# Kernel optimization log

Measured on AMD Instinct MI355X. Metric: run time of the kernel, lower is better.

The kernel has to match this reference:

```python
import jax, jax.numpy as jnp
import numpy as np

D, NH = 1024, 16
B, L = 2, 2048
NEG = -1e9


def setup_inputs() -> dict:
    key = jax.random.key(0)
    ks = jax.random.split(key, 6)
    x = jax.random.normal(ks[0], (B, L, D), dtype=jnp.float32)
    # causal additive mask, broadcast over batch and heads
    causal = jnp.tril(jnp.ones((L, L), dtype=jnp.float32))
    mask = jnp.where(causal == 1.0, 0.0, NEG)[None, None, :, :]
    wx_w = jax.random.normal(ks[1], (3 * D, D), dtype=jnp.float32) * 0.02
    wx_b = jnp.zeros((3 * D,), dtype=jnp.float32)
    wo_w = jax.random.normal(ks[2], (D, D), dtype=jnp.float32) * 0.02
    wo_b = jnp.zeros((D,), dtype=jnp.float32)
    ln_g = jnp.ones((D,), dtype=jnp.float32)
    ln_b = jnp.zeros((D,), dtype=jnp.float32)
    return {"x": x, "mask": mask, "wx_w": wx_w, "wx_b": wx_b,
            "wo_w": wo_w, "wo_b": wo_b, "ln_g": ln_g, "ln_b": ln_b}


def _layernorm(x, g, b, eps=1e-5):
    mu = jnp.mean(x, axis=-1, keepdims=True)
    var = jnp.mean((x - mu) ** 2, axis=-1, keepdims=True)
    return (x - mu) * jax.lax.rsqrt(var + eps) * g + b


def reference(x, mask, wx_w, wx_b, wo_w, wo_b, ln_g, ln_b):
    b, l, d = x.shape
    nh = NH
    dh = d // nh
    h = _layernorm(x, ln_g, ln_b)
    proj = h @ wx_w.T + wx_b                       # [b, l, 3d]
    # 'b l (n nh dh) -> n b nh l dh'
    proj = proj.reshape(b, l, 3, nh, dh)
    q, k, v = jnp.moveaxis(proj, 2, 0).transpose(0, 1, 3, 2, 4)  # each [b, nh, l, dh]
    qkT = jnp.einsum('bhic,bhjc->bhij', q, k) + mask
    scale = jnp.asarray(d, jnp.float32) ** 0.5     # NOTE: sqrt(d), not sqrt(dh)
    attn = jax.nn.softmax(qkT / scale, axis=-1)
    heads = jnp.einsum('bhij,bhjc->bhic', attn, v)  # [b, nh, l, dh]
    heads = heads.transpose(0, 2, 1, 3).reshape(b, l, d)
    attention = heads @ wo_w.T + wo_b
    out = jax.nn.gelu(x + attention, approximate=False)
    return (out, mask)
```

## Files before the change

kernel.cpp:

```cpp
#include <hip/hip_runtime.h>
#include <hip/hip_bf16.h>
#include <math.h>

constexpr int kD  = 1024;
constexpr int kB  = 2;
constexpr int kL  = 2048;
constexpr int kM  = kB * kL;

typedef __attribute__((ext_vector_type(8))) short  bf8v;
typedef __attribute__((ext_vector_type(4))) float  f4v;
typedef __attribute__((ext_vector_type(4))) unsigned short us4v;

#define MFMA_BF16 __builtin_amdgcn_mfma_f32_16x16x32_bf16

__device__ inline unsigned short f2bf(float f) {
    __hip_bfloat16 h = __float2bfloat16(f);
    return *(unsigned short*)&h;
}
__device__ inline float bf2f(unsigned short u) {
    __hip_bfloat16 h = *(__hip_bfloat16*)&u;
    return __bfloat162float(h);
}
__device__ inline void gload16(const void* g, void* l) {
    __builtin_amdgcn_global_load_lds(
        (const __attribute__((address_space(1))) void*)g,
        (__attribute__((address_space(3))) void*)l, 16, 0, 0);
}

__global__ __launch_bounds__(256) void convert_split(
    const float* __restrict__ src, unsigned short* __restrict__ hi,
    unsigned short* __restrict__ lo, int n4)
{
    const int i = blockIdx.x * 256 + threadIdx.x;
    if (i >= n4) return;
    const float4 v = ((const float4*)src)[i];
    const float vv[4] = {v.x, v.y, v.z, v.w};
    us4v h, l;
    #pragma unroll
    for (int c = 0; c < 4; ++c) {
        h[c] = f2bf(vv[c]);
        l[c] = f2bf(vv[c] - bf2f(h[c]));
    }
    *(us4v*)&hi[(size_t)i * 4] = h;
    *(us4v*)&lo[(size_t)i * 4] = l;
}

__global__ __launch_bounds__(256) void ln_kernel(
    const float* __restrict__ x, const float* __restrict__ g,
    const float* __restrict__ beta, unsigned short* __restrict__ h_hi,
    unsigned short* __restrict__ h_lo)
{
    const int row = blockIdx.x;
    const int tid = threadIdx.x;
    const float4 v = ((const float4*)(x + (size_t)row * kD))[tid];
    float s  = v.x + v.y + v.z + v.w;
    float s2 = v.x*v.x + v.y*v.y + v.z*v.z + v.w*v.w;
    #pragma unroll
    for (int off = 32; off > 0; off >>= 1) {
        s  += __shfl_down(s, off);
        s2 += __shfl_down(s2, off);
    }
    __shared__ float wsum[4], wsum2[4];
    const int lane = tid & 63, wid = tid >> 6;
    if (lane == 0) { wsum[wid] = s; wsum2[wid] = s2; }
    __syncthreads();
    const float ts   = wsum[0] + wsum[1] + wsum[2] + wsum[3];
    const float ts2  = wsum2[0] + wsum2[1] + wsum2[2] + wsum2[3];
    const float mean = ts * (1.0f / kD);
    const float var  = ts2 * (1.0f / kD) - mean * mean;
    const float rstd = rsqrtf(var + 1e-5f);
    const float4 gv = ((const float4*)g)[tid];
    const float4 bv = ((const float4*)beta)[tid];
    float o[4];
    o[0] = (v.x - mean) * rstd * gv.x + bv.x;
    o[1] = (v.y - mean) * rstd * gv.y + bv.y;
    o[2] = (v.z - mean) * rstd * gv.z + bv.z;
    o[3] = (v.w - mean) * rstd * gv.w + bv.w;
    us4v h, l;
    #pragma unroll
    for (int c = 0; c < 4; ++c) {
        h[c] = f2bf(o[c]);
        l[c] = f2bf(o[c] - bf2f(h[c]));
    }
    *(us4v*)&h_hi[(size_t)row * kD + tid * 4] = h;
    *(us4v*)&h_lo[(size_t)row * kD + tid * 4] = l;
}

template<int MODE>
__global__ __launch_bounds__(256, 3) void gemm_split(
    const unsigned short* __restrict__ Ahi, const unsigned short* __restrict__ Alo,
    const unsigned short* __restrict__ Bhi, const unsigned short* __restrict__ Blo,
    const float* __restrict__ bias, const float* __restrict__ resid,
    unsigned short* __restrict__ outb, unsigned short* __restrict__ vT,
    float* __restrict__ outf, int N, int K)
{
    constexpr int NARR = (MODE == 0) ? 4 : 3;
    __shared__ unsigned short S[NARR][128][32];
    const int tid = threadIdx.x;
    const int l = tid & 63, w = tid >> 6;
    const int col16 = l & 15, grp = l >> 4;
    const int wr = (w >> 1) * 64, wc = (w & 1) * 64;
    const int row0 = blockIdx.y * 128, col0 = blockIdx.x * 128;
    const int sr = l >> 2;
    const int sc8 = ((l & 3) ^ ((sr >> 1) & 3)) * 8;
    const unsigned short* gb;
    int rb;
    if (MODE == 0) {
        gb = (w == 0) ? Ahi : (w == 1) ? Alo : (w == 2) ? Bhi : Blo;
        rb = (w < 2) ? row0 : col0;
    } else {
        gb = (w == 0) ? Ahi : (w == 1) ? Bhi : Blo;
        rb = (w == 0) ? row0 : col0;
    }
    const bool do_stage = (MODE == 0) || (w < 3);
    const int pos8 = (grp ^ ((col16 >> 1) & 3)) * 8;
    f4v acc[4][4] = {};

    for (int k0 = 0; k0 < K; k0 += 32) {
        __syncthreads();
        if (do_stage) {
            #pragma unroll
            for (int t = 0; t < 8; ++t)
                gload16(gb + (size_t)(rb + t*16 + sr) * K + k0 + sc8,
                        &S[w][t*16][0]);
        }
        __syncthreads();
        bf8v ah[4], al[4], bh[4], bl[4];
        #pragma unroll
        for (int mi = 0; mi < 4; ++mi) {
            ah[mi] = *(bf8v*)&S[0][wr + mi*16 + col16][pos8];
            if (MODE == 0) al[mi] = *(bf8v*)&S[1][wr + mi*16 + col16][pos8];
        }
        #pragma unroll
        for (int ni = 0; ni < 4; ++ni) {
            bh[ni] = *(bf8v*)&S[(MODE == 0) ? 2 : 1][wc + ni*16 + col16][pos8];
            bl[ni] = *(bf8v*)&S[(MODE == 0) ? 3 : 2][wc + ni*16 + col16][pos8];
        }
        #pragma unroll
        for (int mi = 0; mi < 4; ++mi)
            #pragma unroll
            for (int ni = 0; ni < 4; ++ni) {
                acc[mi][ni] = MFMA_BF16(ah[mi], bh[ni], acc[mi][ni], 0, 0, 0);
                acc[mi][ni] = MFMA_BF16(ah[mi], bl[ni], acc[mi][ni], 0, 0, 0);
                if (MODE == 0)
                    acc[mi][ni] = MFMA_BF16(al[mi], bh[ni], acc[mi][ni], 0, 0, 0);
            }
    }
    #pragma unroll
    for (int mi = 0; mi < 4; ++mi)
        #pragma unroll
        for (int ni = 0; ni < 4; ++ni) {
            const int gcol = col0 + wc + ni*16 + col16;
            const float bb = bias[gcol];
            #pragma unroll
            for (int rr = 0; rr < 4; ++rr) {
                const int grow = row0 + wr + mi*16 + grp*4 + rr;
                float o = acc[mi][ni][rr] + bb;
                if (MODE == 0) {
                    if (gcol < 2048) {
                        if (gcol < 1024) o *= (1.0f / 32.0f);
                        outb[(size_t)grow * 3072 + gcol] = f2bf(o);
                    } else {
                        const int dg = gcol - 2048;
                        vT[((size_t)((grow >> 11) * 16 + (dg >> 6)) * 64 + (dg & 63)) * 2048
                           + (grow & 2047)] = f2bf(o);
                    }
                } else {
                    o += resid[(size_t)grow * N + gcol];
                    o = 0.5f * o * (1.0f + erff(o * 0.70710678118654752f));
                    outf[(size_t)grow * N + gcol] = o;
                }
            }
        }
}

__global__ __launch_bounds__(256, 4) void attn_mfma(
    const unsigned short* __restrict__ projb, const unsigned short* __restrict__ vT,
    unsigned short* __restrict__ heads_hi)
{
    __shared__ unsigned short Ks[64 * 64];
    __shared__ unsigned short Vs[64 * 64];
    __shared__ unsigned int   Ps32[4][16][68];
    const int tid = threadIdx.x;
    const int l = tid & 63, w = tid >> 6;
    const int col16 = l & 15, grp = l >> 4;
    const int bh = blockIdx.x, b = bh >> 4, hh = bh & 15;
    const int qt = 31 - (int)blockIdx.y;
    const int q0 = qt * 64;
    const unsigned short* vTh = vT + (size_t)bh * 64 * 2048;

    const int r8 = l >> 3;
    const int sc8 = ((l & 7) ^ r8) * 8;
    const int isV = w >> 1;
    const int t0 = (w & 1) * 4;
    const int sw7 = col16 & 7;

    const size_t qbase = (size_t)(b*kL + q0 + w*16 + col16) * 3072 + hh*64 + grp*8;
    bf8v aq[2];
    aq[0] = *(const bf8v*)&projb[qbase];
    aq[1] = *(const bf8v*)&projb[qbase + 32];

    f4v accO[4] = {};
    float m_r[4], l_r[4];
    #pragma unroll
    for (int r = 0; r < 4; ++r) { m_r[r] = -INFINITY; l_r[r] = 0.0f; }

    for (int jt = 0; jt <= qt; ++jt) {
        const int j0 = jt * 64;
        __syncthreads();
        #pragma unroll
        for (int t2 = 0; t2 < 4; ++t2) {
            const int t = t0 + t2;
            if (isV)
                gload16(&vTh[(size_t)(t*8 + r8) * 2048 + j0 + sc8], &Vs[t*8*64]);
            else
                gload16(&projb[(size_t)(b*kL + j0 + t*8 + r8) * 3072 + hh*64 + 1024 + sc8],
                        &Ks[t*8*64]);
        }
        __syncthreads();

        f4v accS[4] = {};
        #pragma unroll
        for (int kk = 0; kk < 2; ++kk)
            #pragma unroll
            for (int nj = 0; nj < 4; ++nj) {
                const int row = nj*16 + col16;
                const bf8v bk = *(bf8v*)&Ks[row*64 + (((grp + kk*4) ^ sw7) * 8)];
                accS[nj] = MFMA_BF16(aq[kk], bk, accS[nj], 0, 0, 0);
            }

        const bool diag = (jt == qt);
        float p[4][4];
        float alpha[4];
        #pragma unroll
        for (int r = 0; r < 4; ++r) {
            const int q_local = w*16 + grp*4 + r;
            float sv[4];
            #pragma unroll
            for (int nj = 0; nj < 4; ++nj) {
                sv[nj] = accS[nj][r];
                if (diag && (nj*16 + col16 > q_local)) sv[nj] = -1e9f;
            }
            float pm = fmaxf(fmaxf(sv[0], sv[1]), fmaxf(sv[2], sv[3]));
            pm = fmaxf(pm, __shfl_xor(pm, 1));
            pm = fmaxf(pm, __shfl_xor(pm, 2));
            pm = fmaxf(pm, __shfl_xor(pm, 4));
            pm = fmaxf(pm, __shfl_xor(pm, 8));
            const float m_new = fmaxf(m_r[r], pm);
            alpha[r] = __expf(m_r[r] - m_new);
            m_r[r] = m_new;
            float ps = 0.0f;
            #pragma unroll
            for (int nj = 0; nj < 4; ++nj) {
                p[nj][r] = __expf(sv[nj] - m_new);
                ps += p[nj][r];
            }
            ps += __shfl_xor(ps, 1);
            ps += __shfl_xor(ps, 2);
            ps += __shfl_xor(ps, 4);
            ps += __shfl_xor(ps, 8);
            l_r[r] = l_r[r] * alpha[r] + ps;
        }
        #pragma unroll
        for (int nd = 0; nd < 4; ++nd)
            #pragma unroll
            for (int r = 0; r < 4; ++r)
                accO[nd][r] *= alpha[r];

        #pragma unroll
        for (int nj = 0; nj < 4; ++nj)
            #pragma unroll
            for (int r = 0; r < 4; ++r) {
                const unsigned hi = f2bf(p[nj][r]);
                const unsigned lo = f2bf(p[nj][r] - bf2f((unsigned short)hi));
                Ps32[w][grp*4 + r][nj*16 + col16] = hi | (lo << 16);
            }
        asm volatile("s_waitcnt lgkmcnt(0)" ::: "memory");

        #pragma unroll
        for (int js = 0; js < 2; ++js) {
            const uint4 pa0 = *(const uint4*)&Ps32[w][col16][js*32 + grp*8];
            const uint4 pa1 = *(const uint4*)&Ps32[w][col16][js*32 + grp*8 + 4];
            const unsigned pu[8] = {pa0.x, pa0.y, pa0.z, pa0.w,
                                    pa1.x, pa1.y, pa1.z, pa1.w};
            bf8v ph, pl;
            #pragma unroll
            for (int i = 0; i < 8; ++i) {
                ph[i] = (short)(pu[i] & 0xffffu);
                pl[i] = (short)(pu[i] >> 16);
            }
            #pragma unroll
            for (int nd = 0; nd < 4; ++nd) {
                const int row = nd*16 + col16;
                const bf8v bv = *(bf8v*)&Vs[row*64 + (((grp + js*4) ^ sw7) * 8)];
                accO[nd] = MFMA_BF16(ph, bv, accO[nd], 0, 0, 0);
                accO[nd] = MFMA_BF16(pl, bv, accO[nd], 0, 0, 0);
            }
        }
    }
    #pragma unroll
    for (int nd = 0; nd < 4; ++nd)
        #pragma unroll
        for (int r = 0; r < 4; ++r) {
            const float o = accO[nd][r] / l_r[r];
            heads_hi[(size_t)(b*kL + q0 + w*16 + grp*4 + r) * kD
                     + hh*64 + nd*16 + col16] = f2bf(o);
        }
}

extern "C" void kernel_launch(void* const* d_in, const int* in_sizes, int n_in,
                              void* d_out, int out_size, void* d_ws, size_t ws_size,
                              hipStream_t stream)
{
    const float* x    = (const float*)d_in[0];
    const float* mask = (const float*)d_in[1];
    const float* wx_w = (const float*)d_in[2];
    const float* wx_b = (const float*)d_in[3];
    const float* wo_w = (const float*)d_in[4];
    const float* wo_b = (const float*)d_in[5];
    const float* ln_g = (const float*)d_in[6];
    const float* ln_b = (const float*)d_in[7];
    float* out = (float*)d_out;

    unsigned short* h_hi  = (unsigned short*)d_ws;
    unsigned short* h_lo  = h_hi  + (size_t)kM * kD;
    unsigned short* wxhi  = h_lo  + (size_t)kM * kD;
    unsigned short* wxlo  = wxhi  + (size_t)3 * kD * kD;
    unsigned short* wohi  = wxlo  + (size_t)3 * kD * kD;
    unsigned short* wolo  = wohi  + (size_t)kD * kD;
    unsigned short* projb = wolo  + (size_t)kD * kD;
    unsigned short* hd_hi = projb + (size_t)kM * 3 * kD;
    unsigned short* vT    = hd_hi + (size_t)kM * kD;

    convert_split<<<(3*kD*kD/4 + 255)/256, 256, 0, stream>>>(wx_w, wxhi, wxlo, 3*kD*kD/4);
    convert_split<<<(kD*kD/4 + 255)/256, 256, 0, stream>>>(wo_w, wohi, wolo, kD*kD/4);
    ln_kernel<<<kM, 256, 0, stream>>>(x, ln_g, ln_b, h_hi, h_lo);
    gemm_split<0><<<dim3(3*kD/128, kM/128), 256, 0, stream>>>(
        h_hi, h_lo, wxhi, wxlo, wx_b, nullptr, projb, vT, nullptr, 3*kD, kD);
    attn_mfma<<<dim3(kB*16, kL/64), 256, 0, stream>>>(projb, vT, hd_hi);
    gemm_split<1><<<dim3(kD/128, kM/128), 256, 0, stream>>>(
        hd_hi, nullptr, wohi, wolo, wo_b, x, nullptr, nullptr, out, kD, kD);
    hipMemcpyAsync(out + (size_t)kM * kD, mask, (size_t)kL * kL * sizeof(float),
                   hipMemcpyDeviceToDevice, stream);
}
```

Baseline: 314.2 us.

## Double GEMM K-tile to 64 and use 128-row query tiles in attention

The split-bf16 GEMM now stages 64-wide K slices per barrier pair, which halves the number of sync/load rounds and changes the LDS swizzle to an 8-way XOR pattern. Occupancy for the QKV GEMM is lowered because it now uses more shared memory. The attention kernel switches to 512-thread blocks covering 128 query rows, so each staged K/V tile is shared by 8 waves instead of 4. Waves whose rows lie entirely before the last key tile skip that tile. The trade-off is fewer resident blocks and larger per-block LDS, plus coarser causal load balance.

```diff
diff --git a/kernel.cpp b/kernel.cpp
--- a/kernel.cpp
+++ b/kernel.cpp
@@ -87,7 +87,7 @@
 }
 
 template<int MODE>
-__global__ __launch_bounds__(256, 3) void gemm_split(
+__global__ __launch_bounds__(256, (MODE == 0) ? 2 : 3) void gemm_split(
     const unsigned short* __restrict__ Ahi, const unsigned short* __restrict__ Alo,
     const unsigned short* __restrict__ Bhi, const unsigned short* __restrict__ Blo,
     const float* __restrict__ bias, const float* __restrict__ resid,
@@ -95,14 +95,14 @@
     float* __restrict__ outf, int N, int K)
 {
     constexpr int NARR = (MODE == 0) ? 4 : 3;
-    __shared__ unsigned short S[NARR][128][32];
+    __shared__ unsigned short S[NARR][128][64];
     const int tid = threadIdx.x;
     const int l = tid & 63, w = tid >> 6;
     const int col16 = l & 15, grp = l >> 4;
     const int wr = (w >> 1) * 64, wc = (w & 1) * 64;
     const int row0 = blockIdx.y * 128, col0 = blockIdx.x * 128;
-    const int sr = l >> 2;
-    const int sc8 = ((l & 3) ^ ((sr >> 1) & 3)) * 8;
+    const int sr8 = l >> 3;
+    const int sc8 = ((l & 7) ^ sr8) * 8;
     const unsigned short* gb;
     int rb;
     if (MODE == 0) {
@@ -113,38 +113,42 @@
         rb = (w == 0) ? row0 : col0;
     }
     const bool do_stage = (MODE == 0) || (w < 3);
-    const int pos8 = (grp ^ ((col16 >> 1) & 3)) * 8;
+    const int sw7 = col16 & 7;
     f4v acc[4][4] = {};
 
-    for (int k0 = 0; k0 < K; k0 += 32) {
+    for (int k0 = 0; k0 < K; k0 += 64) {
         __syncthreads();
         if (do_stage) {
             #pragma unroll
-            for (int t = 0; t < 8; ++t)
-                gload16(gb + (size_t)(rb + t*16 + sr) * K + k0 + sc8,
-                        &S[w][t*16][0]);
+            for (int t = 0; t < 16; ++t)
+                gload16(gb + (size_t)(rb + t*8 + sr8) * K + k0 + sc8,
+                        &S[w][t*8][0]);
         }
         __syncthreads();
-        bf8v ah[4], al[4], bh[4], bl[4];
         #pragma unroll
-        for (int mi = 0; mi < 4; ++mi) {
-            ah[mi] = *(bf8v*)&S[0][wr + mi*16 + col16][pos8];
-            if (MODE == 0) al[mi] = *(bf8v*)&S[1][wr + mi*16 + col16][pos8];
-        }
-        #pragma unroll
-        for (int ni = 0; ni < 4; ++ni) {
-            bh[ni] = *(bf8v*)&S[(MODE == 0) ? 2 : 1][wc + ni*16 + col16][pos8];
-            bl[ni] = *(bf8v*)&S[(MODE == 0) ? 3 : 2][wc + ni*16 + col16][pos8];
-        }
-        #pragma unroll
-        for (int mi = 0; mi < 4; ++mi)
+        for (int kk = 0; kk < 2; ++kk) {
+            const int pos8 = ((grp + kk*4) ^ sw7) * 8;
+            bf8v ah[4], al[4], bh[4], bl[4];
+            #pragma unroll
+            for (int mi = 0; mi < 4; ++mi) {
+                ah[mi] = *(bf8v*)&S[0][wr + mi*16 + col16][pos8];
+                if (MODE == 0) al[mi] = *(bf8v*)&S[1][wr + mi*16 + col16][pos8];
+            }
             #pragma unroll
             for (int ni = 0; ni < 4; ++ni) {
-                acc[mi][ni] = MFMA_BF16(ah[mi], bh[ni], acc[mi][ni], 0, 0, 0);
-                acc[mi][ni] = MFMA_BF16(ah[mi], bl[ni], acc[mi][ni], 0, 0, 0);
-                if (MODE == 0)
-                    acc[mi][ni] = MFMA_BF16(al[mi], bh[ni], acc[mi][ni], 0, 0, 0);
-            }
+                bh[ni] = *(bf8v*)&S[(MODE == 0) ? 2 : 1][wc + ni*16 + col16][pos8];
+                bl[ni] = *(bf8v*)&S[(MODE == 0) ? 3 : 2][wc + ni*16 + col16][pos8];
+            }
+            #pragma unroll
+            for (int mi = 0; mi < 4; ++mi)
+                #pragma unroll
+                for (int ni = 0; ni < 4; ++ni) {
+                    acc[mi][ni] = MFMA_BF16(ah[mi], bh[ni], acc[mi][ni], 0, 0, 0);
+                    acc[mi][ni] = MFMA_BF16(ah[mi], bl[ni], acc[mi][ni], 0, 0, 0);
+                    if (MODE == 0)
+                        acc[mi][ni] = MFMA_BF16(al[mi], bh[ni], acc[mi][ni], 0, 0, 0);
+                }
+        }
     }
     #pragma unroll
     for (int mi = 0; mi < 4; ++mi)
@@ -174,25 +178,25 @@
         }
 }
 
-__global__ __launch_bounds__(256, 4) void attn_mfma(
+__global__ __launch_bounds__(512, 6) void attn_mfma(
     const unsigned short* __restrict__ projb, const unsigned short* __restrict__ vT,
     unsigned short* __restrict__ heads_hi)
 {
     __shared__ unsigned short Ks[64 * 64];
     __shared__ unsigned short Vs[64 * 64];
-    __shared__ unsigned int   Ps32[4][16][68];
+    __shared__ unsigned int   Ps32[8][16][68];
     const int tid = threadIdx.x;
     const int l = tid & 63, w = tid >> 6;
     const int col16 = l & 15, grp = l >> 4;
     const int bh = blockIdx.x, b = bh >> 4, hh = bh & 15;
-    const int qt = 31 - (int)blockIdx.y;
-    const int q0 = qt * 64;
+    const int qt = 15 - (int)blockIdx.y;
+    const int q0 = qt * 128;
     const unsigned short* vTh = vT + (size_t)bh * 64 * 2048;
 
     const int r8 = l >> 3;
     const int sc8 = ((l & 7) ^ r8) * 8;
-    const int isV = w >> 1;
-    const int t0 = (w & 1) * 4;
+    const bool isV = w >= 4;
+    const int tA = (w & 3) * 2;
     const int sw7 = col16 & 7;
 
     const size_t qbase = (size_t)(b*kL + q0 + w*16 + col16) * 3072 + hh*64 + grp*8;
@@ -205,12 +209,13 @@
     #pragma unroll
     for (int r = 0; r < 4; ++r) { m_r[r] = -INFINITY; l_r[r] = 0.0f; }
 
-    for (int jt = 0; jt <= qt; ++jt) {
+    const int ntiles = 2 * qt + 2;
+    for (int jt = 0; jt < ntiles; ++jt) {
         const int j0 = jt * 64;
         __syncthreads();
         #pragma unroll
-        for (int t2 = 0; t2 < 4; ++t2) {
-            const int t = t0 + t2;
+        for (int t2 = 0; t2 < 2; ++t2) {
+            const int t = tA + t2;
             if (isV)
                 gload16(&vTh[(size_t)(t*8 + r8) * 2048 + j0 + sc8], &Vs[t*8*64]);
             else
@@ -219,82 +224,84 @@
         }
         __syncthreads();
 
-        f4v accS[4] = {};
-        #pragma unroll
-        for (int kk = 0; kk < 2; ++kk)
-            #pragma unroll
-            for (int nj = 0; nj < 4; ++nj) {
-                const int row = nj*16 + col16;
-                const bf8v bk = *(bf8v*)&Ks[row*64 + (((grp + kk*4) ^ sw7) * 8)];
-                accS[nj] = MFMA_BF16(aq[kk], bk, accS[nj], 0, 0, 0);
-            }
-
-        const bool diag = (jt == qt);
-        float p[4][4];
-        float alpha[4];
-        #pragma unroll
-        for (int r = 0; r < 4; ++r) {
-            const int q_local = w*16 + grp*4 + r;
-            float sv[4];
-            #pragma unroll
-            for (int nj = 0; nj < 4; ++nj) {
-                sv[nj] = accS[nj][r];
-                if (diag && (nj*16 + col16 > q_local)) sv[nj] = -1e9f;
-            }
-            float pm = fmaxf(fmaxf(sv[0], sv[1]), fmaxf(sv[2], sv[3]));
-            pm = fmaxf(pm, __shfl_xor(pm, 1));
-            pm = fmaxf(pm, __shfl_xor(pm, 2));
-            pm = fmaxf(pm, __shfl_xor(pm, 4));
-            pm = fmaxf(pm, __shfl_xor(pm, 8));
-            const float m_new = fmaxf(m_r[r], pm);
-            alpha[r] = __expf(m_r[r] - m_new);
-            m_r[r] = m_new;
-            float ps = 0.0f;
-            #pragma unroll
-            for (int nj = 0; nj < 4; ++nj) {
-                p[nj][r] = __expf(sv[nj] - m_new);
-                ps += p[nj][r];
-            }
-            ps += __shfl_xor(ps, 1);
-            ps += __shfl_xor(ps, 2);
-            ps += __shfl_xor(ps, 4);
-            ps += __shfl_xor(ps, 8);
-            l_r[r] = l_r[r] * alpha[r] + ps;
-        }
-        #pragma unroll
-        for (int nd = 0; nd < 4; ++nd)
-            #pragma unroll
-            for (int r = 0; r < 4; ++r)
-                accO[nd][r] *= alpha[r];
-
-        #pragma unroll
-        for (int nj = 0; nj < 4; ++nj)
+        if (!((jt == 2*qt + 1) && (w < 4))) {
+            f4v accS[4] = {};
+            #pragma unroll
+            for (int kk = 0; kk < 2; ++kk)
+                #pragma unroll
+                for (int nj = 0; nj < 4; ++nj) {
+                    const int row = nj*16 + col16;
+                    const bf8v bk = *(bf8v*)&Ks[row*64 + (((grp + kk*4) ^ sw7) * 8)];
+                    accS[nj] = MFMA_BF16(aq[kk], bk, accS[nj], 0, 0, 0);
+                }
+
+            const int joff = (jt - 2*qt) * 64;
+            float p[4][4];
+            float alpha[4];
             #pragma unroll
             for (int r = 0; r < 4; ++r) {
-                const unsigned hi = f2bf(p[nj][r]);
-                const unsigned lo = f2bf(p[nj][r] - bf2f((unsigned short)hi));
-                Ps32[w][grp*4 + r][nj*16 + col16] = hi | (lo << 16);
-            }
-        asm volatile("s_waitcnt lgkmcnt(0)" ::: "memory");
-
-        #pragma unroll
-        for (int js = 0; js < 2; ++js) {
-            const uint4 pa0 = *(const uint4*)&Ps32[w][col16][js*32 + grp*8];
-            const uint4 pa1 = *(const uint4*)&Ps32[w][col16][js*32 + grp*8 + 4];
-            const unsigned pu[8] = {pa0.x, pa0.y, pa0.z, pa0.w,
-                                    pa1.x, pa1.y, pa1.z, pa1.w};
-            bf8v ph, pl;
-            #pragma unroll
-            for (int i = 0; i < 8; ++i) {
-                ph[i] = (short)(pu[i] & 0xffffu);
-                pl[i] = (short)(pu[i] >> 16);
-            }
-            #pragma unroll
-            for (int nd = 0; nd < 4; ++nd) {
-                const int row = nd*16 + col16;
-                const bf8v bv = *(bf8v*)&Vs[row*64 + (((grp + js*4) ^ sw7) * 8)];
-                accO[nd] = MFMA_BF16(ph, bv, accO[nd], 0, 0, 0);
-                accO[nd] = MFMA_BF16(pl, bv, accO[nd], 0, 0, 0);
+                const int qloc = w*16 + grp*4 + r;
+                float sv[4];
+                #pragma unroll
+                for (int nj = 0; nj < 4; ++nj) {
+                    sv[nj] = accS[nj][r];
+                    if (joff + nj*16 + col16 > qloc) sv[nj] = -1e9f;
+                }
+                float pm = fmaxf(fmaxf(sv[0], sv[1]), fmaxf(sv[2], sv[3]));
+                pm = fmaxf(pm, __shfl_xor(pm, 1));
+                pm = fmaxf(pm, __shfl_xor(pm, 2));
+                pm = fmaxf(pm, __shfl_xor(pm, 4));
+                pm = fmaxf(pm, __shfl_xor(pm, 8));
+                const float m_new = fmaxf(m_r[r], pm);
+                alpha[r] = __expf(m_r[r] - m_new);
+                m_r[r] = m_new;
+                float ps = 0.0f;
+                #pragma unroll
+                for (int nj = 0; nj < 4; ++nj) {
+                    p[nj][r] = __expf(sv[nj] - m_new);
+                    ps += p[nj][r];
+                }
+                ps += __shfl_xor(ps, 1);
+                ps += __shfl_xor(ps, 2);
+                ps += __shfl_xor(ps, 4);
+                ps += __shfl_xor(ps, 8);
+                l_r[r] = l_r[r] * alpha[r] + ps;
+            }
+            #pragma unroll
+            for (int nd = 0; nd < 4; ++nd)
+                #pragma unroll
+                for (int r = 0; r < 4; ++r)
+                    accO[nd][r] *= alpha[r];
+
+            #pragma unroll
+            for (int nj = 0; nj < 4; ++nj)
+                #pragma unroll
+                for (int r = 0; r < 4; ++r) {
+                    const unsigned hi = f2bf(p[nj][r]);
+                    const unsigned lo = f2bf(p[nj][r] - bf2f((unsigned short)hi));
+                    Ps32[w][grp*4 + r][nj*16 + col16] = hi | (lo << 16);
+                }
+            asm volatile("s_waitcnt lgkmcnt(0)" ::: "memory");
+
+            #pragma unroll
+            for (int js = 0; js < 2; ++js) {
+                const uint4 pa0 = *(const uint4*)&Ps32[w][col16][js*32 + grp*8];
+                const uint4 pa1 = *(const uint4*)&Ps32[w][col16][js*32 + grp*8 + 4];
+                const unsigned pu[8] = {pa0.x, pa0.y, pa0.z, pa0.w,
+                                        pa1.x, pa1.y, pa1.z, pa1.w};
+                bf8v ph, pl;
+                #pragma unroll
+                for (int i = 0; i < 8; ++i) {
+                    ph[i] = (short)(pu[i] & 0xffffu);
+                    pl[i] = (short)(pu[i] >> 16);
+                }
+                #pragma unroll
+                for (int nd = 0; nd < 4; ++nd) {
+                    const int row = nd*16 + col16;
+                    const bf8v bv = *(bf8v*)&Vs[row*64 + (((grp + js*4) ^ sw7) * 8)];
+                    accO[nd] = MFMA_BF16(ph, bv, accO[nd], 0, 0, 0);
+                    accO[nd] = MFMA_BF16(pl, bv, accO[nd], 0, 0, 0);
+                }
             }
         }
     }
@@ -337,7 +344,7 @@
     ln_kernel<<<kM, 256, 0, stream>>>(x, ln_g, ln_b, h_hi, h_lo);
     gemm_split<0><<<dim3(3*kD/128, kM/128), 256, 0, stream>>>(
         h_hi, h_lo, wxhi, wxlo, wx_b, nullptr, projb, vT, nullptr, 3*kD, kD);
-    attn_mfma<<<dim3(kB*16, kL/64), 256, 0, stream>>>(projb, vT, hd_hi);
+    attn_mfma<<<dim3(kB*16, kL/128), 512, 0, stream>>>(projb, vT, hd_hi);
     gemm_split<1><<<dim3(kD/128, kM/128), 256, 0, stream>>>(
         hd_hi, nullptr, wohi, wolo, wo_b, x, nullptr, nullptr, out, kD, kD);
     hipMemcpyAsync(out + (size_t)kM * kD, mask, (size_t)kL * kL * sizeof(float),
```

New measurement: 340.4 us. 8.4% more time.
